# Kernel optimization log

Hardware: AMD Instinct MI355X
Metric: run time of the kernel (lower is better)

Reference implementation:

```python
import jax, jax.numpy as jnp
import numpy as np

DIM = 24
HID = 256
N = 4096
NUM_LO = DIM * (DIM - 1) // 2  # 276
NEG = -0.01  # slope used in the hand-written Jacobians (source uses -0.01, NOT the fwd leaky slope 0.01; faithful)


def _linear_params(key, out_dim, in_dim):
    kw, kb = jax.random.split(key)
    s = 1.0 / np.sqrt(in_dim)
    W = jax.random.uniform(kw, (out_dim, in_dim), jnp.float32, -s, s)
    b = jax.random.uniform(kb, (out_dim,), jnp.float32, -s, s)
    return W, b


def setup_inputs() -> dict:
    key = jax.random.key(0)
    k = jax.random.split(key, 7)
    W1, b1 = _linear_params(k[0], HID, DIM)
    W2, b2 = _linear_params(k[1], HID, HID)
    WG, bG = _linear_params(k[2], DIM, HID)
    WLd, bLd = _linear_params(k[3], DIM, HID)
    WLo, bLo = _linear_params(k[4], NUM_LO, HID)
    q = jax.random.normal(k[5], (N, DIM), jnp.float32)
    q_dot = jax.random.normal(k[6], (N, DIM), jnp.float32)
    return {"q": q, "q_dot": q_dot, "W1": W1, "b1": b1, "W2": W2, "b2": b2,
            "WG": WG, "bG": bG, "WLd": WLd, "bLd": bLd, "WLo": WLo, "bLo": bLo}


def _forward(q, q_dot, W1, b1, W2, b2, WG, bG, WLd, bLd, WLo, bLo):
    n, d = q.shape
    tr, tc = np.tril_indices(d, -1)  # row-major strict-lower order == torch mask-flatten order
    di = np.arange(d)
    # MLP trunk (torch leaky_relu default slope 0.01)
    h1 = jax.nn.leaky_relu(q @ W1.T + b1)                       # [n,HID]
    h2 = jax.nn.leaky_relu(h1 @ W2.T + b2)                      # [n,HID]
    h3 = h2 @ WLd.T + bLd                                       # [n,d]
    g = h2 @ WG.T + bG                                          # [n,d]
    Ld = jax.nn.softplus(h3)                                    # [n,d]
    Lo = h2 @ WLo.T + bLo                                       # [n,NUM_LO]
    # Lower-triangular L (diag_embed(Ld) + masked strict-lower fill)
    L = jnp.zeros((n, d, d), q.dtype).at[:, tr, tc].set(Lo).at[:, di, di].set(Ld)
    # Hand-written Jacobian chain; diag_embed(v)@W == v[:,:,None]*W (direct elementwise scaling)
    dR1 = jnp.where(h1 > 0, 1.0, NEG)
    J1 = dR1[:, :, None] * W1                                    # dh1/dq  [n,HID,d]
    dR2 = jnp.where(h2 > 0, 1.0, NEG)
    J2 = dR2[:, :, None] * jnp.einsum('ij,njd->nid', W2, J1)     # dh2/dq  [n,HID,d]
    sig = jax.nn.sigmoid(h3)
    dld_dq = sig[:, :, None] * jnp.einsum('ij,njd->nid', WLd, J2)  # [n,d,d]
    dlo_dq = jnp.einsum('oj,njd->nod', WLo, J2)                  # [n,NUM_LO,d]
    dld_dt = jnp.einsum('nid,nd->ni', dld_dq, q_dot)             # [n,d]
    dlo_dt = jnp.einsum('nod,nd->no', dlo_dq, q_dot)             # [n,NUM_LO]
    dL_dt = jnp.zeros((n, d, d), q.dtype).at[:, tr, tc].set(dlo_dt).at[:, di, di].set(dld_dt)
    # 4D assembly: torch does L[L==1] = dlo_dq.view(-1), which reinterprets the (lo, q_idx)
    # flat buffer in (q_idx, tril_pos) order -> plain reshape replicates that exactly.
    vals = dlo_dq.reshape(n, d, NUM_LO)
    dld_dq_p = dld_dq.transpose(0, 2, 1)                         # [n, d_q, d_ld]
    dL_dq = jnp.zeros((n, d, d, d), q.dtype).at[:, :, tr, tc].set(vals).at[:, :, di, di].set(dld_dq_p)
    eye = jnp.eye(d, dtype=q.dtype)
    M = L @ L.transpose(0, 2, 1) + 1e-9 * eye
    dM_dt = L @ dL_dt.transpose(0, 2, 1) + dL_dt @ L.transpose(0, 2, 1)
    # Quadratic term. torch: q_dot.repeat(d,1)/L.repeat(d,1,1) index as (i % n) while
    # dL_dq.view(n*d,d,d) indexes as (i // d, i % d) -> replicate exactly (faithful).
    idx = jnp.arange(n * d) % n
    qd_r = q_dot[idx]                                            # [n*d, d]
    L_r = L[idx]                                                 # [n*d, d, d]
    dL_i = dL_dq.reshape(n * d, d, d)
    S = dL_i @ L_r.transpose(0, 2, 1) + L_r @ dL_i.transpose(0, 2, 1)
    quad = jnp.einsum('bi,bij,bj->b', qd_r, S, qd_r).reshape(n, d)
    c = jnp.einsum('nij,nj->ni', dM_dt, q_dot) - 0.5 * quad
    return M, c, g


def reference(q, q_dot, W1, b1, W2, b2, WG, bG, WLd, bLd, WLo, bLo):
    return _forward(q, q_dot, W1, b1, W2, b2, WG, bG, WLd, bLd, WLo, bLo)
```

## Files before the change

### kernel.cpp

```cpp
#include <hip/hip_runtime.h>
#include <math.h>

#define DIM 24
#define HID 256
#define NLO 276
#define NSAMP 4096
#define C_OFF 2359296
#define G_OFF 2457600

#define OFF_W2FH 0
#define OFF_W2FL 32768
#define OFF_WEFH 65536
#define OFF_WEFL 106496
#define OFF_W1H16 147456
#define OFF_W1L16 151552
#define OFF_W2H16 155648
#define OFF_W2L16 188416
#define OFF_WHH16 221184
#define OFF_WHL16 264192
#define OFF_MSKT 307200
#define OFF_SIGT 372736
#define OFF_LDT  471040
#define OFF_UT   569344
#define OFF_LOT  667648

typedef __attribute__((ext_vector_type(8))) short bf16x8;
typedef __attribute__((ext_vector_type(8))) _Float16 f16x8;
typedef __attribute__((ext_vector_type(4))) float f32x4;

__device__ __forceinline__ float leaky(float x){ return x > 0.f ? x : 0.01f*x; }
__device__ __forceinline__ unsigned short f2b(float f){
  unsigned u = __float_as_uint(f);
  return (unsigned short)((u + 0x7FFFu + ((u >> 16) & 1u)) >> 16);
}
__device__ __forceinline__ float b2f(unsigned short h){ return __uint_as_float(((unsigned)h) << 16); }
__device__ __forceinline__ void f2h2(float v, unsigned short* hi, unsigned short* lo){
  _Float16 h = (_Float16)v;
  _Float16 l = (_Float16)((v - (float)h) * 4096.f);
  *hi = *(unsigned short*)&h; *lo = *(unsigned short*)&l;
}

__global__ __launch_bounds__(256) void k0_prep(
    const float* __restrict__ W1, const float* __restrict__ W2,
    const float* __restrict__ WG, const float* __restrict__ WLd,
    const float* __restrict__ WLo, float* __restrict__ ws)
{
  const int tid = blockIdx.x*256 + threadIdx.x;
  const int nth = gridDim.x*256;
  unsigned short* W2FH = (unsigned short*)(ws + OFF_W2FH);
  unsigned short* W2FL = (unsigned short*)(ws + OFF_W2FL);
  for (int e = tid; e < 65536; e += nth){
    int j=e&7, l=(e>>3)&63, kb=(e>>9)&7, mt=e>>12;
    int m = mt*16+(l&15), k = kb*32+((l>>4)&3)*8+j;
    float v = W2[m*256+k];
    unsigned short h = f2b(v);
    W2FH[e]=h; W2FL[e]=f2b(v-b2f(h));
  }
  unsigned short* WEFH = (unsigned short*)(ws + OFF_WEFH);
  unsigned short* WEFL = (unsigned short*)(ws + OFF_WEFL);
  for (int e = tid; e < 81920; e += nth){
    int j=e&7, l=(e>>3)&63, kb=(e>>9)&7, mt=e>>12;
    int r = mt*16+(l&15), k = kb*32+((l>>4)&3)*8+j;
    float v = 0.f;
    if (r < 24) v = WLd[r*256+k]; else if (r < 300) v = WLo[(r-24)*256+k];
    unsigned short h = f2b(v);
    WEFH[e]=h; WEFL[e]=f2b(v-b2f(h));
  }
  unsigned short* W1H = (unsigned short*)(ws + OFF_W1H16);
  unsigned short* W1L = (unsigned short*)(ws + OFF_W1L16);
  for (int e = tid; e < 8192; e += nth){
    int j=e&7, l=(e>>3)&63, mt=e>>9;
    int m = mt*16+(l&15), k = ((l>>4)&3)*8+j;
    float v = (k < 24) ? W1[m*24+k] : 0.f;
    f2h2(v, &W1H[e], &W1L[e]);
  }
  unsigned short* W2H = (unsigned short*)(ws + OFF_W2H16);
  unsigned short* W2L = (unsigned short*)(ws + OFF_W2L16);
  for (int e = tid; e < 65536; e += nth){
    int j=e&7, l=(e>>3)&63, kb=(e>>9)&7, mt=e>>12;
    int m = mt*16+(l&15), k = kb*32+((l>>4)&3)*8+j;
    f2h2(W2[m*256+k], &W2H[e], &W2L[e]);
  }
  unsigned short* WHH = (unsigned short*)(ws + OFF_WHH16);
  unsigned short* WHL = (unsigned short*)(ws + OFF_WHL16);
  for (int e = tid; e < 86016; e += nth){
    int j=e&7, l=(e>>3)&63, kb=(e>>9)&7, mt=e>>12;
    int rr = mt*16+(l&15), k = kb*32+((l>>4)&3)*8+j;
    float v = 0.f;
    if (rr < 24) v = WLd[rr*256+k];
    else if (rr < 48) v = WG[(rr-24)*256+k];
    else if (rr < 324) v = WLo[(rr-48)*256+k];
    f2h2(v, &WHH[e], &WHL[e]);
  }
}

__global__ __launch_bounds__(256) void k1_fwd(
    const float* __restrict__ q, const float* __restrict__ qd_g,
    const float* __restrict__ b1, const float* __restrict__ b2,
    const float* __restrict__ bG, const float* __restrict__ bLd,
    const float* __restrict__ bLo, float* __restrict__ ws,
    float* __restrict__ out)
{
  const int s0 = blockIdx.x*4, t = threadIdx.x;
  const int w = t>>6, l = t&63, l15 = l&15, l4g = (l>>4)&3;
  unsigned* MSKT = (unsigned*)(ws + OFF_MSKT);
  float* SIGT = ws + OFF_SIGT;
  float* LDT  = ws + OFF_LDT;
  float* UT   = ws + OFF_UT;
  float* LOT  = ws + OFF_LOT;

  __shared__ __align__(16) unsigned short pool[8448];
  __shared__ unsigned char mb[4][64];
  __shared__ float qd_s[4][24];
  __shared__ float Lsm[4][600];
  unsigned short* BQH = pool;
  unsigned short* BQL = BQH + 160;
  unsigned short* BH2 = pool;
  unsigned short* BL2 = BH2 + 4224;

  for (int f = t; f < 96; f += 256){
    float v = q[s0*24 + f];
    int n = f/24, k = f%24;
    f2h2(v, &BQH[n*40+k], &BQL[n*40+k]);
    ((float*)qd_s)[f] = qd_g[s0*24 + f];
  }
  if (t < 32){ int n = t>>3, k = 24 + (t&7); BQH[n*40+k]=0; BQL[n*40+k]=0; }
  __syncthreads();

  f32x4 aH[4], aX[4];
  #pragma unroll
  for (int i=0;i<4;++i){ aH[i]=(f32x4){0,0,0,0}; aX[i]=(f32x4){0,0,0,0}; }
  {
    const f16x8* WH = (const f16x8*)(ws + OFF_W1H16);
    const f16x8* WL = (const f16x8*)(ws + OFF_W1L16);
    f16x8 Af[4], Al[4];
    #pragma unroll
    for (int i=0;i<4;++i){ int mt=w+4*i; Af[i]=WH[mt*64+l]; Al[i]=WL[mt*64+l]; }
    int off = l15*40 + l4g*8;
    f16x8 Bh = *(const f16x8*)(BQH+off), Bl = *(const f16x8*)(BQL+off);
    #pragma unroll
    for (int i=0;i<4;++i){
      aH[i]=__builtin_amdgcn_mfma_f32_16x16x32_f16(Af[i],Bh,aH[i],0,0,0);
      aX[i]=__builtin_amdgcn_mfma_f32_16x16x32_f16(Af[i],Bl,aX[i],0,0,0);
      aX[i]=__builtin_amdgcn_mfma_f32_16x16x32_f16(Al[i],Bh,aX[i],0,0,0);
    }
  }
  __syncthreads();
  #pragma unroll
  for (int i=0;i<4;++i){
    int m0=(w+4*i)*16+4*l4g;
    float4 bb = *(const float4*)(b1+m0);
    int n = l15;
    if (n < 4){
      unsigned nib=0; unsigned short hs[4], ls[4];
      #pragma unroll
      for (int r=0;r<4;++r){
        float val = aH[i][r] + aX[i][r]*(1.f/4096.f) + ((const float*)&bb)[r];
        if (val > 0.f) nib |= 1u<<r;
        f2h2(leaky(val), &hs[r], &ls[r]);
      }
      mb[n][(m0>>2)] = (unsigned char)nib;
      *(uint2*)(BH2 + n*264 + m0) = make_uint2((unsigned)hs[0]|((unsigned)hs[1]<<16),
                                               (unsigned)hs[2]|((unsigned)hs[3]<<16));
      *(uint2*)(BL2 + n*264 + m0) = make_uint2((unsigned)ls[0]|((unsigned)ls[1]<<16),
                                               (unsigned)ls[2]|((unsigned)ls[3]<<16));
    }
  }
  __syncthreads();
  if (t < 32){
    int n = t&3, w8 = t>>2; unsigned word = 0;
    #pragma unroll
    for (int b=0;b<8;++b) word |= (unsigned)(mb[n][w8*8+b] & 0xFu) << (4*b);
    MSKT[w8*NSAMP + s0+n] = word;
  }

  #pragma unroll
  for (int i=0;i<4;++i){ aH[i]=(f32x4){0,0,0,0}; aX[i]=(f32x4){0,0,0,0}; }
  {
    const f16x8* WH = (const f16x8*)(ws + OFF_W2H16);
    const f16x8* WL = (const f16x8*)(ws + OFF_W2L16);
    for (int kb=0;kb<8;++kb){
      f16x8 Af[4], Al[4];
      #pragma unroll
      for (int i=0;i<4;++i){ int mt=w+4*i; Af[i]=WH[(mt*8+kb)*64+l]; Al[i]=WL[(mt*8+kb)*64+l]; }
      int off = l15*264 + kb*32 + l4g*8;
      f16x8 Bh = *(const f16x8*)(BH2+off), Bl = *(const f16x8*)(BL2+off);
      #pragma unroll
      for (int i=0;i<4;++i){
        aH[i]=__builtin_amdgcn_mfma_f32_16x16x32_f16(Af[i],Bh,aH[i],0,0,0);
        aX[i]=__builtin_amdgcn_mfma_f32_16x16x32_f16(Af[i],Bl,aX[i],0,0,0);
        aX[i]=__builtin_amdgcn_mfma_f32_16x16x32_f16(Al[i],Bh,aX[i],0,0,0);
      }
    }
  }
  __syncthreads();
  #pragma unroll
  for (int i=0;i<4;++i){
    int m0=(w+4*i)*16+4*l4g;
    float4 bb = *(const float4*)(b2+m0);
    int n = l15;
    if (n < 4){
      unsigned nib=0; unsigned short hs[4], ls[4];
      #pragma unroll
      for (int r=0;r<4;++r){
        float val = aH[i][r] + aX[i][r]*(1.f/4096.f) + ((const float*)&bb)[r];
        if (val > 0.f) nib |= 1u<<r;
        f2h2(leaky(val), &hs[r], &ls[r]);
      }
      mb[n][(m0>>2)] = (unsigned char)nib;
      *(uint2*)(BH2 + n*264 + m0) = make_uint2((unsigned)hs[0]|((unsigned)hs[1]<<16),
                                               (unsigned)hs[2]|((unsigned)hs[3]<<16));
      *(uint2*)(BL2 + n*264 + m0) = make_uint2((unsigned)ls[0]|((unsigned)ls[1]<<16),
                                               (unsigned)ls[2]|((unsigned)ls[3]<<16));
    }
  }
  __syncthreads();
  if (t < 32){
    int n = t&3, w8 = t>>2; unsigned word = 0;
    #pragma unroll
    for (int b=0;b<8;++b) word |= (unsigned)(mb[n][w8*8+b] & 0xFu) << (4*b);
    MSKT[(8+w8)*NSAMP + s0+n] = word;
  }

  for (int pass=0; pass<2; ++pass){
    f32x4 cH[3], cX[3];
    #pragma unroll
    for (int i=0;i<3;++i){ cH[i]=(f32x4){0,0,0,0}; cX[i]=(f32x4){0,0,0,0}; }
    const f16x8* WH = (const f16x8*)(ws + OFF_WHH16);
    const f16x8* WL = (const f16x8*)(ws + OFF_WHL16);
    for (int kb=0;kb<8;++kb){
      f16x8 Af[3], Al[3];
      #pragma unroll
      for (int i=0;i<3;++i){
        int mt = w + 4*(3*pass+i);
        if (mt < 21){ Af[i]=WH[(mt*8+kb)*64+l]; Al[i]=WL[(mt*8+kb)*64+l]; }
      }
      int off = l15*264 + kb*32 + l4g*8;
      f16x8 Bh = *(const f16x8*)(BH2+off), Bl = *(const f16x8*)(BL2+off);
      #pragma unroll
      for (int i=0;i<3;++i){
        int mt = w + 4*(3*pass+i);
        if (mt < 21){
          cH[i]=__builtin_amdgcn_mfma_f32_16x16x32_f16(Af[i],Bh,cH[i],0,0,0);
          cX[i]=__builtin_amdgcn_mfma_f32_16x16x32_f16(Af[i],Bl,cX[i],0,0,0);
          cX[i]=__builtin_amdgcn_mfma_f32_16x16x32_f16(Al[i],Bh,cX[i],0,0,0);
        }
      }
    }
    #pragma unroll
    for (int i=0;i<3;++i){
      int mt = w + 4*(3*pass+i);
      if (mt >= 21) continue;
      int m0 = mt*16+4*l4g;
      int n = l15;
      if (n < 4){
        int sG = s0+n;
        int tr = 0, tc = 0;
        if (m0 >= 48){
          int p = m0 - 48;
          tr = (int)((1.f + sqrtf(1.f + 8.f*(float)p))*0.5f);
          while (tr*(tr-1)/2 > p) --tr;
          while ((tr+1)*tr/2 <= p) ++tr;
          tc = p - tr*(tr-1)/2;
        }
        #pragma unroll
        for (int r=0;r<4;++r){
          int rr = m0+r;
          float val = cH[i][r] + cX[i][r]*(1.f/4096.f);
          if (rr < 24){
            val += bLd[rr];
            SIGT[rr*NSAMP + sG] = 1.f/(1.f + expf(-val));
            float sp = fmaxf(val,0.f) + log1pf(expf(-fabsf(val)));
            LDT[rr*NSAMP + sG] = sp;
            Lsm[n][rr*25 + rr] = sp;
          } else if (rr < 48){
            out[G_OFF + sG*24 + (rr-24)] = val + bG[rr-24];
          } else if (rr < 324){
            float lov = val + bLo[rr-48];
            LOT[(rr-48)*NSAMP + sG] = lov;
            Lsm[n][tr*25 + tc] = lov;
            if (++tc == tr){ ++tr; tc = 0; }
          }
        }
      }
    }
  }
  __syncthreads();

  for (int n2 = 0; n2 < 4; ++n2){
    const float* Ls = Lsm[n2];
    for (int e = t; e < 576; e += 256){
      int r = e/24, c = e%24, km = min(r,c);
      float acc = (r == c) ? 1e-9f : 0.f;
      for (int k = 0; k <= km; ++k) acc += Ls[r*25+k]*Ls[c*25+k];
      out[(size_t)(s0+n2)*576 + e] = acc;
    }
  }
  if (t < 96){
    int n = t/24, c = t%24;
    float u = qd_s[n][c]*Lsm[n][c*25+c];
    for (int r = c+1; r < 24; ++r) u += qd_s[n][r]*Lsm[n][r*25+c];
    UT[c*NSAMP + s0+n] = u;
  }
}

__global__ __launch_bounds__(256, 3) void kDE(
    const float* __restrict__ q_dot, const float* __restrict__ W1g,
    float* __restrict__ ws, float* __restrict__ out)
{
  const int n0 = blockIdx.x*2, t = threadIdx.x;
  const int w = t >> 6, l = t & 63;
  const int l15 = l & 15, l4g = (l >> 4) & 3;
  const unsigned* MSKT = (const unsigned*)(ws + OFF_MSKT);
  const float* SIGT = ws + OFF_SIGT;
  const float* LDT  = ws + OFF_LDT;
  const float* UT   = ws + OFF_UT;
  const float* LOT  = ws + OFF_LOT;

  __shared__ __align__(16) char pool[50688];
  __shared__ unsigned msk[2][16];
  unsigned short* BH = (unsigned short*)pool;
  unsigned short* BL = BH + 12672;
  float* dlo_flat = (float*)pool;
  float* dld25    = (float*)(pool + 26496);
  float* qdm_s    = (float*)(pool + 28896);
  float* um_s     = (float*)(pool + 31296);
  float* qp2      = (float*)(pool + 33696);
  float* dtlo     = (float*)(pool + 40320);
  float* dtld     = (float*)(pool + 41424);
  float* w1s      = (float*)(pool + 41520);
  float* sigs     = (float*)(pool + 41616);
  float* qds      = (float*)(pool + 41712);
  float* uss      = (float*)(pool + 41808);
  float* qps      = (float*)(pool + 41904);

  if (t < 32) msk[t>>4][t&15] = MSKT[(t&15)*NSAMP + n0 + (t>>4)];
  __syncthreads();

  {
    float w1r[24];
    #pragma unroll
    for (int d = 0; d < 24; ++d) w1r[d] = W1g[t*24 + d];
    float dr0 = ((msk[0][t>>5] >> (t&31)) & 1u) ? 1.f : -0.01f;
    float dr1 = ((msk[1][t>>5] >> (t&31)) & 1u) ? 1.f : -0.01f;
    #pragma unroll
    for (int c = 0; c < 48; ++c){
      int s = c >= 24, d = c - 24*s;
      float f = (s ? dr1 : dr0) * w1r[d];
      unsigned short h = f2b(f);
      BH[c*264 + t] = h;
      BL[c*264 + t] = f2b(f - b2f(h));
    }
  }
  __syncthreads();

  f32x4 accD[4][3];
  #pragma unroll
  for (int i = 0; i < 4; ++i)
    #pragma unroll
    for (int nt = 0; nt < 3; ++nt) accD[i][nt] = (f32x4){0.f,0.f,0.f,0.f};
  {
    const bf16x8* AHp = (const bf16x8*)(ws + OFF_W2FH);
    const bf16x8* ALp = (const bf16x8*)(ws + OFF_W2FL);
    for (int kb = 0; kb < 8; ++kb){
      bf16x8 AH[4], AL[4], BHf[3], BLf[3];
      #pragma unroll
      for (int i = 0; i < 4; ++i){
        int mt = 4*w + i;
        AH[i] = AHp[(mt*8+kb)*64 + l];
        AL[i] = ALp[(mt*8+kb)*64 + l];
      }
      #pragma unroll
      for (int nt = 0; nt < 3; ++nt){
        int off = (nt*16 + l15)*264 + kb*32 + l4g*8;
        BHf[nt] = *(const bf16x8*)(BH + off);
        BLf[nt] = *(const bf16x8*)(BL + off);
      }
      #pragma unroll
      for (int i = 0; i < 4; ++i)
        #pragma unroll
        for (int nt = 0; nt < 3; ++nt){
          accD[i][nt] = __builtin_amdgcn_mfma_f32_16x16x32_bf16(AH[i], BHf[nt], accD[i][nt], 0, 0, 0);
          accD[i][nt] = __builtin_amdgcn_mfma_f32_16x16x32_bf16(AH[i], BLf[nt], accD[i][nt], 0, 0, 0);
          accD[i][nt] = __builtin_amdgcn_mfma_f32_16x16x32_bf16(AL[i], BHf[nt], accD[i][nt], 0, 0, 0);
        }
    }
  }
  __syncthreads();

  #pragma unroll
  for (int i = 0; i < 4; ++i){
    int mt = 4*w + i;
    int m0 = mt*16 + 4*l4g;
    int bb = m0 & 31;
    #pragma unroll
    for (int nt = 0; nt < 3; ++nt){
      int c = nt*16 + l15;
      int s = c >= 24;
      unsigned word = msk[s][8 + (mt>>1)];
      unsigned uh[4], ul[4];
      #pragma unroll
      for (int r = 0; r < 4; ++r){
        float sc = ((word >> (bb + r)) & 1u) ? 1.f : -0.01f;
        float v = sc * accD[i][nt][r];
        unsigned uv = __float_as_uint(v);
        uh[r] = uv;
        float lo = v - __uint_as_float(uv & 0xFFFF0000u);
        ul[r] = __float_as_uint(lo);
      }
      *(uint2*)(BH + c*264 + m0) = make_uint2((uh[0]>>16) | (uh[1] & 0xFFFF0000u),
                                              (uh[2]>>16) | (uh[3] & 0xFFFF0000u));
      *(uint2*)(BL + c*264 + m0) = make_uint2((ul[0]>>16) | (ul[1] & 0xFFFF0000u),
                                              (ul[2]>>16) | (ul[3] & 0xFFFF0000u));
    }
  }
  __syncthreads();

  f32x4 accE[5][3];
  #pragma unroll
  for (int i = 0; i < 5; ++i)
    #pragma unroll
    for (int nt = 0; nt < 3; ++nt) accE[i][nt] = (f32x4){0.f,0.f,0.f,0.f};
  {
    const bf16x8* AHp = (const bf16x8*)(ws + OFF_WEFH);
    const bf16x8* ALp = (const bf16x8*)(ws + OFF_WEFL);
    for (int kb = 0; kb < 8; ++kb){
      bf16x8 AH[5], AL[5], BHf[3], BLf[3];
      #pragma unroll
      for (int i = 0; i < 5; ++i){
        int mt = 5*w + i;
        AH[i] = AHp[(mt*8+kb)*64 + l];
        AL[i] = ALp[(mt*8+kb)*64 + l];
      }
      #pragma unroll
      for (int nt = 0; nt < 3; ++nt){
        int off = (nt*16 + l15)*264 + kb*32 + l4g*8;
        BHf[nt] = *(const bf16x8*)(BH + off);
        BLf[nt] = *(const bf16x8*)(BL + off);
      }
      #pragma unroll
      for (int i = 0; i < 5; ++i)
        #pragma unroll
        for (int nt = 0; nt < 3; ++nt){
          accE[i][nt] = __builtin_amdgcn_mfma_f32_16x16x32_bf16(AH[i], BHf[nt], accE[i][nt], 0, 0, 0);
          accE[i][nt] = __builtin_amdgcn_mfma_f32_16x16x32_bf16(AH[i], BLf[nt], accE[i][nt], 0, 0, 0);
          accE[i][nt] = __builtin_amdgcn_mfma_f32_16x16x32_bf16(AL[i], BHf[nt], accE[i][nt], 0, 0, 0);
        }
    }
  }
  __syncthreads();

  for (int s = 0; s < 2; ++s){
    const int n = n0 + s;
    #pragma unroll
    for (int i = 0; i < 5; ++i){
      int mt = 5*w + i;
      #pragma unroll
      for (int nt = 0; nt < 3; ++nt){
        int c = nt*16 + l15;
        if ((c >= 24) == (s == 1)){
          int d = c - 24*s;
          #pragma unroll
          for (int r = 0; r < 4; ++r){
            int re = mt*16 + 4*l4g + r;
            if (re < 24) dld25[re*25 + d] = accE[i][nt][r];
            else if (re < 300) dlo_flat[(re-24)*24 + d] = accE[i][nt][r];
          }
        }
      }
    }
    for (int e = t; e < 576; e += 256){
      int a_ = e/24, b_ = e%24;
      int ma = (n*24 + a_) & (NSAMP-1);
      int mb_ = (n*24 + b_) & (NSAMP-1);
      qdm_s[a_*25 + b_] = q_dot[ma*24 + b_];
      um_s[a_*25 + b_]  = UT[a_*NSAMP + mb_];
    }
    if (t < 24){
      sigs[t] = SIGT[t*NSAMP + n];
      qds[t]  = q_dot[n*24 + t];
      uss[t]  = UT[t*NSAMP + n];
    }
    __syncthreads();

    for (int k = t; k < 1656; k += 256){
      float4 v = *(const float4*)(dlo_flat + 4*k);
      int j4 = (k % 6)*4;
      qp2[k] = v.x*qds[j4] + v.y*qds[j4+1] + v.z*qds[j4+2] + v.w*qds[j4+3];
    }
    if (t < 24){
      float a = 0.f;
      #pragma unroll
      for (int d = 0; d < 24; ++d) a += dld25[t*25+d]*qds[d];
      dtld[t] = sigs[t]*a;
    }
    __syncthreads();

    for (int o = t; o < 276; o += 256){
      float a = 0.f;
      #pragma unroll
      for (int j = 0; j < 6; ++j) a += qp2[o*6+j];
      dtlo[o] = a;
    }
    __syncthreads();

    if (t < 96){
      int g = t/24, i = t%24;
      float part = 0.f;
      for (int c2 = g; c2 < 24; c2 += 4){
        float v = qdm_s[i*25+c2]*sigs[c2]*dld25[c2*25+i];
        for (int r = c2+1; r < 24; ++r){
          int p = r*(r-1)/2 + c2;
          v += qdm_s[i*25+r]*dlo_flat[i*276 + p];
        }
        part += um_s[c2*25+i]*v;
      }
      qps[g*24 + i] = part;
    } else if (t >= 128 && t < 152){
      int i = t - 128;
      float a = qds[i]*dtld[i];
      for (int j = i+1; j < 24; ++j) a += qds[j]*dtlo[j*(j-1)/2 + i];
      w1s[i] = a;
    }
    __syncthreads();

    if (t < 24){
      const int i = t;
      float cs = dtld[i]*uss[i] + LDT[i*NSAMP + n]*w1s[i];
      for (int k = 0; k < i; ++k){
        int p = i*(i-1)/2 + k;
        cs += LOT[p*NSAMP + n]*w1s[k] + dtlo[p]*uss[k];
      }
      float quad = qps[i] + qps[24+i] + qps[48+i] + qps[72+i];
      out[C_OFF + n*24 + i] = cs - quad;
    }
    __syncthreads();
  }
}

extern "C" void kernel_launch(void* const* d_in, const int* in_sizes, int n_in,
                              void* d_out, int out_size, void* d_ws, size_t ws_size,
                              hipStream_t stream)
{
  const float* q   = (const float*)d_in[0];
  const float* qd  = (const float*)d_in[1];
  const float* W1  = (const float*)d_in[2];
  const float* b1  = (const float*)d_in[3];
  const float* W2  = (const float*)d_in[4];
  const float* b2  = (const float*)d_in[5];
  const float* WG  = (const float*)d_in[6];
  const float* bG  = (const float*)d_in[7];
  const float* WLd = (const float*)d_in[8];
  const float* bLd = (const float*)d_in[9];
  const float* WLo = (const float*)d_in[10];
  const float* bLo = (const float*)d_in[11];
  float* out = (float*)d_out;
  float* ws  = (float*)d_ws;

  k0_prep<<<256, 256, 0, stream>>>(W1, W2, WG, WLd, WLo, ws);
  k1_fwd<<<NSAMP/4, 256, 0, stream>>>(q, qd, b1, b2, bG, bLd, bLo, ws, out);
  kDE<<<NSAMP/2, 256, 0, stream>>>(qd, W1, ws, out);
}
```

Baseline: 281.4 us.

## Process 16 samples per block in forward MLP kernel to fill MFMA columns

The forward kernel previously used only 4 of the 16 MFMA N-columns per tile, discarding three quarters of each matrix op. It now handles 16 samples per block with 512 threads (8 waves), so every MFMA column carries a real sample and each weight fragment load is amortized over four times as many samples. Work per wave is re-split across 8 waves, and shared memory grows for the mask, L and q_dot buffers. The grid shrinks to a quarter as many blocks, which may reduce occupancy or parallelism on this small problem.

```diff
diff --git a/kernel.cpp b/kernel.cpp
--- a/kernel.cpp
+++ b/kernel.cpp
@@ -94,14 +94,14 @@
   }
 }
 
-__global__ __launch_bounds__(256) void k1_fwd(
+__global__ __launch_bounds__(512) void k1_fwd(
     const float* __restrict__ q, const float* __restrict__ qd_g,
     const float* __restrict__ b1, const float* __restrict__ b2,
     const float* __restrict__ bG, const float* __restrict__ bLd,
     const float* __restrict__ bLo, float* __restrict__ ws,
     float* __restrict__ out)
 {
-  const int s0 = blockIdx.x*4, t = threadIdx.x;
+  const int s0 = blockIdx.x*16, t = threadIdx.x;
   const int w = t>>6, l = t&63, l15 = l&15, l4g = (l>>4)&3;
   unsigned* MSKT = (unsigned*)(ws + OFF_MSKT);
   float* SIGT = ws + OFF_SIGT;
@@ -110,36 +110,36 @@
   float* LOT  = ws + OFF_LOT;
 
   __shared__ __align__(16) unsigned short pool[8448];
-  __shared__ unsigned char mb[4][64];
-  __shared__ float qd_s[4][24];
-  __shared__ float Lsm[4][600];
+  __shared__ unsigned char mb[16][64];
+  __shared__ float qd_s[16][24];
+  __shared__ float Lsm[16][600];
   unsigned short* BQH = pool;
-  unsigned short* BQL = BQH + 160;
+  unsigned short* BQL = BQH + 640;
   unsigned short* BH2 = pool;
   unsigned short* BL2 = BH2 + 4224;
 
-  for (int f = t; f < 96; f += 256){
-    float v = q[s0*24 + f];
-    int n = f/24, k = f%24;
+  if (t < 384){
+    float v = q[s0*24 + t];
+    int n = t/24, k = t%24;
     f2h2(v, &BQH[n*40+k], &BQL[n*40+k]);
-    ((float*)qd_s)[f] = qd_g[s0*24 + f];
-  }
-  if (t < 32){ int n = t>>3, k = 24 + (t&7); BQH[n*40+k]=0; BQL[n*40+k]=0; }
-  __syncthreads();
-
-  f32x4 aH[4], aX[4];
-  #pragma unroll
-  for (int i=0;i<4;++i){ aH[i]=(f32x4){0,0,0,0}; aX[i]=(f32x4){0,0,0,0}; }
+    ((float*)qd_s)[t] = qd_g[s0*24 + t];
+  }
+  if (t < 256){ int n = t>>4, k = 24 + (t&15); BQH[n*40+k]=0; BQL[n*40+k]=0; }
+  __syncthreads();
+
+  f32x4 aH[2], aX[2];
+  #pragma unroll
+  for (int i=0;i<2;++i){ aH[i]=(f32x4){0,0,0,0}; aX[i]=(f32x4){0,0,0,0}; }
   {
     const f16x8* WH = (const f16x8*)(ws + OFF_W1H16);
     const f16x8* WL = (const f16x8*)(ws + OFF_W1L16);
-    f16x8 Af[4], Al[4];
-    #pragma unroll
-    for (int i=0;i<4;++i){ int mt=w+4*i; Af[i]=WH[mt*64+l]; Al[i]=WL[mt*64+l]; }
+    f16x8 Af[2], Al[2];
+    #pragma unroll
+    for (int i=0;i<2;++i){ int mt=w+8*i; Af[i]=WH[mt*64+l]; Al[i]=WL[mt*64+l]; }
     int off = l15*40 + l4g*8;
     f16x8 Bh = *(const f16x8*)(BQH+off), Bl = *(const f16x8*)(BQL+off);
     #pragma unroll
-    for (int i=0;i<4;++i){
+    for (int i=0;i<2;++i){
       aH[i]=__builtin_amdgcn_mfma_f32_16x16x32_f16(Af[i],Bh,aH[i],0,0,0);
       aX[i]=__builtin_amdgcn_mfma_f32_16x16x32_f16(Af[i],Bl,aX[i],0,0,0);
       aX[i]=__builtin_amdgcn_mfma_f32_16x16x32_f16(Al[i],Bh,aX[i],0,0,0);
@@ -147,46 +147,44 @@
   }
   __syncthreads();
   #pragma unroll
-  for (int i=0;i<4;++i){
-    int m0=(w+4*i)*16+4*l4g;
+  for (int i=0;i<2;++i){
+    int m0=(w+8*i)*16+4*l4g;
     float4 bb = *(const float4*)(b1+m0);
     int n = l15;
-    if (n < 4){
-      unsigned nib=0; unsigned short hs[4], ls[4];
-      #pragma unroll
-      for (int r=0;r<4;++r){
-        float val = aH[i][r] + aX[i][r]*(1.f/4096.f) + ((const float*)&bb)[r];
-        if (val > 0.f) nib |= 1u<<r;
-        f2h2(leaky(val), &hs[r], &ls[r]);
-      }
-      mb[n][(m0>>2)] = (unsigned char)nib;
-      *(uint2*)(BH2 + n*264 + m0) = make_uint2((unsigned)hs[0]|((unsigned)hs[1]<<16),
-                                               (unsigned)hs[2]|((unsigned)hs[3]<<16));
-      *(uint2*)(BL2 + n*264 + m0) = make_uint2((unsigned)ls[0]|((unsigned)ls[1]<<16),
-                                               (unsigned)ls[2]|((unsigned)ls[3]<<16));
-    }
-  }
-  __syncthreads();
-  if (t < 32){
-    int n = t&3, w8 = t>>2; unsigned word = 0;
+    unsigned nib=0; unsigned short hs[4], ls[4];
+    #pragma unroll
+    for (int r=0;r<4;++r){
+      float val = aH[i][r] + aX[i][r]*(1.f/4096.f) + ((const float*)&bb)[r];
+      if (val > 0.f) nib |= 1u<<r;
+      f2h2(leaky(val), &hs[r], &ls[r]);
+    }
+    mb[n][(m0>>2)] = (unsigned char)nib;
+    *(uint2*)(BH2 + n*264 + m0) = make_uint2((unsigned)hs[0]|((unsigned)hs[1]<<16),
+                                             (unsigned)hs[2]|((unsigned)hs[3]<<16));
+    *(uint2*)(BL2 + n*264 + m0) = make_uint2((unsigned)ls[0]|((unsigned)ls[1]<<16),
+                                             (unsigned)ls[2]|((unsigned)ls[3]<<16));
+  }
+  __syncthreads();
+  if (t < 128){
+    int n = t&15, w8 = t>>4; unsigned word = 0;
     #pragma unroll
     for (int b=0;b<8;++b) word |= (unsigned)(mb[n][w8*8+b] & 0xFu) << (4*b);
     MSKT[w8*NSAMP + s0+n] = word;
   }
 
   #pragma unroll
-  for (int i=0;i<4;++i){ aH[i]=(f32x4){0,0,0,0}; aX[i]=(f32x4){0,0,0,0}; }
+  for (int i=0;i<2;++i){ aH[i]=(f32x4){0,0,0,0}; aX[i]=(f32x4){0,0,0,0}; }
   {
     const f16x8* WH = (const f16x8*)(ws + OFF_W2H16);
     const f16x8* WL = (const f16x8*)(ws + OFF_W2L16);
     for (int kb=0;kb<8;++kb){
-      f16x8 Af[4], Al[4];
-      #pragma unroll
-      for (int i=0;i<4;++i){ int mt=w+4*i; Af[i]=WH[(mt*8+kb)*64+l]; Al[i]=WL[(mt*8+kb)*64+l]; }
+      f16x8 Af[2], Al[2];
+      #pragma unroll
+      for (int i=0;i<2;++i){ int mt=w+8*i; Af[i]=WH[(mt*8+kb)*64+l]; Al[i]=WL[(mt*8+kb)*64+l]; }
       int off = l15*264 + kb*32 + l4g*8;
       f16x8 Bh = *(const f16x8*)(BH2+off), Bl = *(const f16x8*)(BL2+off);
       #pragma unroll
-      for (int i=0;i<4;++i){
+      for (int i=0;i<2;++i){
         aH[i]=__builtin_amdgcn_mfma_f32_16x16x32_f16(Af[i],Bh,aH[i],0,0,0);
         aX[i]=__builtin_amdgcn_mfma_f32_16x16x32_f16(Af[i],Bl,aX[i],0,0,0);
         aX[i]=__builtin_amdgcn_mfma_f32_16x16x32_f16(Al[i],Bh,aX[i],0,0,0);
@@ -195,108 +193,92 @@
   }
   __syncthreads();
   #pragma unroll
-  for (int i=0;i<4;++i){
-    int m0=(w+4*i)*16+4*l4g;
+  for (int i=0;i<2;++i){
+    int m0=(w+8*i)*16+4*l4g;
     float4 bb = *(const float4*)(b2+m0);
     int n = l15;
-    if (n < 4){
-      unsigned nib=0; unsigned short hs[4], ls[4];
-      #pragma unroll
-      for (int r=0;r<4;++r){
-        float val = aH[i][r] + aX[i][r]*(1.f/4096.f) + ((const float*)&bb)[r];
-        if (val > 0.f) nib |= 1u<<r;
-        f2h2(leaky(val), &hs[r], &ls[r]);
-      }
-      mb[n][(m0>>2)] = (unsigned char)nib;
-      *(uint2*)(BH2 + n*264 + m0) = make_uint2((unsigned)hs[0]|((unsigned)hs[1]<<16),
-                                               (unsigned)hs[2]|((unsigned)hs[3]<<16));
-      *(uint2*)(BL2 + n*264 + m0) = make_uint2((unsigned)ls[0]|((unsigned)ls[1]<<16),
-                                               (unsigned)ls[2]|((unsigned)ls[3]<<16));
-    }
-  }
-  __syncthreads();
-  if (t < 32){
-    int n = t&3, w8 = t>>2; unsigned word = 0;
+    unsigned nib=0; unsigned short hs[4], ls[4];
+    #pragma unroll
+    for (int r=0;r<4;++r){
+      float val = aH[i][r] + aX[i][r]*(1.f/4096.f) + ((const float*)&bb)[r];
+      if (val > 0.f) nib |= 1u<<r;
+      f2h2(leaky(val), &hs[r], &ls[r]);
+    }
+    mb[n][(m0>>2)] = (unsigned char)nib;
+    *(uint2*)(BH2 + n*264 + m0) = make_uint2((unsigned)hs[0]|((unsigned)hs[1]<<16),
+                                             (unsigned)hs[2]|((unsigned)hs[3]<<16));
+    *(uint2*)(BL2 + n*264 + m0) = make_uint2((unsigned)ls[0]|((unsigned)ls[1]<<16),
+                                             (unsigned)ls[2]|((unsigned)ls[3]<<16));
+  }
+  __syncthreads();
+  if (t < 128){
+    int n = t&15, w8 = t>>4; unsigned word = 0;
     #pragma unroll
     for (int b=0;b<8;++b) word |= (unsigned)(mb[n][w8*8+b] & 0xFu) << (4*b);
     MSKT[(8+w8)*NSAMP + s0+n] = word;
   }
 
-  for (int pass=0; pass<2; ++pass){
-    f32x4 cH[3], cX[3];
-    #pragma unroll
-    for (int i=0;i<3;++i){ cH[i]=(f32x4){0,0,0,0}; cX[i]=(f32x4){0,0,0,0}; }
+  for (int pass=0; pass<3; ++pass){
+    int mt = w + 8*pass;
+    bool act = (mt < 21);
+    f32x4 cH=(f32x4){0,0,0,0}, cX=(f32x4){0,0,0,0};
     const f16x8* WH = (const f16x8*)(ws + OFF_WHH16);
     const f16x8* WL = (const f16x8*)(ws + OFF_WHL16);
     for (int kb=0;kb<8;++kb){
-      f16x8 Af[3], Al[3];
-      #pragma unroll
-      for (int i=0;i<3;++i){
-        int mt = w + 4*(3*pass+i);
-        if (mt < 21){ Af[i]=WH[(mt*8+kb)*64+l]; Al[i]=WL[(mt*8+kb)*64+l]; }
-      }
+      f16x8 Af, Al;
+      if (act){ Af=WH[(mt*8+kb)*64+l]; Al=WL[(mt*8+kb)*64+l]; }
       int off = l15*264 + kb*32 + l4g*8;
       f16x8 Bh = *(const f16x8*)(BH2+off), Bl = *(const f16x8*)(BL2+off);
-      #pragma unroll
-      for (int i=0;i<3;++i){
-        int mt = w + 4*(3*pass+i);
-        if (mt < 21){
-          cH[i]=__builtin_amdgcn_mfma_f32_16x16x32_f16(Af[i],Bh,cH[i],0,0,0);
-          cX[i]=__builtin_amdgcn_mfma_f32_16x16x32_f16(Af[i],Bl,cX[i],0,0,0);
-          cX[i]=__builtin_amdgcn_mfma_f32_16x16x32_f16(Al[i],Bh,cX[i],0,0,0);
+      if (act){
+        cH=__builtin_amdgcn_mfma_f32_16x16x32_f16(Af,Bh,cH,0,0,0);
+        cX=__builtin_amdgcn_mfma_f32_16x16x32_f16(Af,Bl,cX,0,0,0);
+        cX=__builtin_amdgcn_mfma_f32_16x16x32_f16(Al,Bh,cX,0,0,0);
+      }
+    }
+    if (act){
+      int m0 = mt*16+4*l4g;
+      int n = l15, sG = s0+n;
+      int tr = 0, tc = 0;
+      if (m0 >= 48){
+        int p = m0 - 48;
+        tr = (int)((1.f + sqrtf(1.f + 8.f*(float)p))*0.5f);
+        while (tr*(tr-1)/2 > p) --tr;
+        while ((tr+1)*tr/2 <= p) ++tr;
+        tc = p - tr*(tr-1)/2;
+      }
+      #pragma unroll
+      for (int r=0;r<4;++r){
+        int rr = m0+r;
+        float val = cH[r] + cX[r]*(1.f/4096.f);
+        if (rr < 24){
+          val += bLd[rr];
+          SIGT[rr*NSAMP + sG] = 1.f/(1.f + expf(-val));
+          float sp = fmaxf(val,0.f) + log1pf(expf(-fabsf(val)));
+          LDT[rr*NSAMP + sG] = sp;
+          Lsm[n][rr*25 + rr] = sp;
+        } else if (rr < 48){
+          out[G_OFF + sG*24 + (rr-24)] = val + bG[rr-24];
+        } else if (rr < 324){
+          float lov = val + bLo[rr-48];
+          LOT[(rr-48)*NSAMP + sG] = lov;
+          Lsm[n][tr*25 + tc] = lov;
+          if (++tc == tr){ ++tr; tc = 0; }
         }
       }
     }
-    #pragma unroll
-    for (int i=0;i<3;++i){
-      int mt = w + 4*(3*pass+i);
-      if (mt >= 21) continue;
-      int m0 = mt*16+4*l4g;
-      int n = l15;
-      if (n < 4){
-        int sG = s0+n;
-        int tr = 0, tc = 0;
-        if (m0 >= 48){
-          int p = m0 - 48;
-          tr = (int)((1.f + sqrtf(1.f + 8.f*(float)p))*0.5f);
-          while (tr*(tr-1)/2 > p) --tr;
-          while ((tr+1)*tr/2 <= p) ++tr;
-          tc = p - tr*(tr-1)/2;
-        }
-        #pragma unroll
-        for (int r=0;r<4;++r){
-          int rr = m0+r;
-          float val = cH[i][r] + cX[i][r]*(1.f/4096.f);
-          if (rr < 24){
-            val += bLd[rr];
-            SIGT[rr*NSAMP + sG] = 1.f/(1.f + expf(-val));
-            float sp = fmaxf(val,0.f) + log1pf(expf(-fabsf(val)));
-            LDT[rr*NSAMP + sG] = sp;
-            Lsm[n][rr*25 + rr] = sp;
-          } else if (rr < 48){
-            out[G_OFF + sG*24 + (rr-24)] = val + bG[rr-24];
-          } else if (rr < 324){
-            float lov = val + bLo[rr-48];
-            LOT[(rr-48)*NSAMP + sG] = lov;
-            Lsm[n][tr*25 + tc] = lov;
-            if (++tc == tr){ ++tr; tc = 0; }
-          }
-        }
-      }
-    }
-  }
-  __syncthreads();
-
-  for (int n2 = 0; n2 < 4; ++n2){
+  }
+  __syncthreads();
+
+  for (int n2 = 0; n2 < 16; ++n2){
     const float* Ls = Lsm[n2];
-    for (int e = t; e < 576; e += 256){
+    for (int e = t; e < 576; e += 512){
       int r = e/24, c = e%24, km = min(r,c);
       float acc = (r == c) ? 1e-9f : 0.f;
       for (int k = 0; k <= km; ++k) acc += Ls[r*25+k]*Ls[c*25+k];
       out[(size_t)(s0+n2)*576 + e] = acc;
     }
   }
-  if (t < 96){
+  if (t < 384){
     int n = t/24, c = t%24;
     float u = qd_s[n][c]*Lsm[n][c*25+c];
     for (int r = c+1; r < 24; ++r) u += qd_s[n][r]*Lsm[n][r*25+c];
@@ -558,6 +540,6 @@
   float* ws  = (float*)d_ws;
 
   k0_prep<<<256, 256, 0, stream>>>(W1, W2, WG, WLd, WLo, ws);
-  k1_fwd<<<NSAMP/4, 256, 0, stream>>>(q, qd, b1, b2, bG, bLd, bLo, ws, out);
+  k1_fwd<<<NSAMP/16, 512, 0, stream>>>(q, qd, b1, b2, bG, bLd, bLo, ws, out);
   kDE<<<NSAMP/2, 256, 0, stream>>>(qd, W1, ws, out);
 }
```

Result: faster. 243.7 us (-13.4%).
